# Performance work log

Measured on AMD Instinct MI355X. Metric: run time of the kernel, lower is better.

## Reference

```python
import jax, jax.numpy as jnp
import numpy as np

B, T, H, W, C = 16, 64, 32, 32, 64
DECAY_V = 0.8
VTH_BASE = 0.5

@jax.custom_vjp
def spike_fn(x, alpha):
    return jnp.where(x > 0, 1.0, 0.0)

def _spike_fwd(x, alpha):
    return spike_fn(x, alpha), (x, alpha)

def _spike_bwd(res, g):
    x, alpha = res
    # fast-sigmoid (SuperSpike) surrogate gradient
    surr = 1.0 / (1.0 + alpha * jnp.abs(x)) ** 2
    return (g * surr, jnp.zeros_like(alpha))

spike_fn.defvjp(_spike_fwd, _spike_bwd)


def setup_inputs() -> dict:
    key = jax.random.key(0)
    k0, k1 = jax.random.split(key, 2)
    x = jax.random.normal(k0, (B, T, H, W, C), dtype=jnp.float32)
    # learned params, shapes = x.shape[2:], matching flax initializers
    step_w_raw = jnp.ones((H, W, C), jnp.float32)                      # nn.initializers.ones
    decay_w_raw = 0.1 * jax.random.normal(k1, (H, W, C), jnp.float32)  # normal(stddev=0.1)
    gamma = jnp.ones((H, W, C), jnp.float32)
    beta = jnp.zeros((H, W, C), jnp.float32)
    return {
        "x": x,
        "hp_alpha": jnp.float32(3.0),
        "hp_base_step": jnp.float32(0.1),
        "hp_base_decay": jnp.float32(0.9),
        "step_w_raw": step_w_raw,
        "decay_w_raw": decay_w_raw,
        "gamma": gamma,
        "beta": beta,
    }


def reference(x, hp_alpha, hp_base_step, hp_base_decay, step_w_raw, decay_w_raw, gamma, beta):
    x_seq = jnp.moveaxis(x, 1, 0)  # [T, B, H, W, C]
    step_w = jax.nn.softplus(step_w_raw)
    decay_w = jax.nn.sigmoid(decay_w_raw)
    # time-invariant effective params (hoisted out of scan; same math as original)
    step_eff = hp_base_step * step_w
    decay_eff = hp_base_decay + (1.0 - hp_base_decay) * decay_w

    def scan_fn(state, x_t):
        v, vth_dyn = state
        v = v * DECAY_V + (x_t * gamma + beta)
        vth_eff = VTH_BASE + vth_dyn
        s = spike_fn(v - vth_eff, hp_alpha)
        v_next = v - vth_eff * jax.lax.stop_gradient(s)
        vth_dyn_next = vth_dyn * decay_eff + jax.lax.stop_gradient(s) * step_eff
        return (v_next, vth_dyn_next), (s, v)

    z = jnp.zeros_like(x_seq[0])
    _, (spikes, voltages) = jax.lax.scan(scan_fn, (z, z), x_seq)
    return jnp.moveaxis(spikes, 0, 1), jnp.moveaxis(voltages, 0, 1)
```

## Files before the change

### kernel.cpp

```cpp
#include <hip/hip_runtime.h>
#include <math.h>

constexpr int Bc = 16, Tc = 64, Hc = 32, Wc = 32, Cc = 64;
constexpr int HWC = Hc * Wc * Cc;
constexpr long long NELEM = (long long)Bc * Tc * HWC;
constexpr float DECAY_V = 0.8f;
constexpr float VTH_BASE = 0.5f;

__global__ __launch_bounds__(256) void alif_fwd_kernel(
    const float* __restrict__ x,
    const float* __restrict__ hp_base_step,
    const float* __restrict__ hp_base_decay,
    const float* __restrict__ step_w_raw,
    const float* __restrict__ decay_w_raw,
    const float* __restrict__ gamma,
    const float* __restrict__ beta,
    float* __restrict__ spikes,
    float* __restrict__ volts)
{
    const int tid = blockIdx.x * blockDim.x + threadIdx.x;
    const int c4  = tid << 2;
    const int b   = c4 >> 16;
    const int hwc = c4 & (HWC - 1);

    const float base_step  = *hp_base_step;
    const float base_decay = *hp_base_decay;

    const float4 swr = *(const float4*)(step_w_raw  + hwc);
    const float4 dwr = *(const float4*)(decay_w_raw + hwc);
    const float4 gm4 = *(const float4*)(gamma       + hwc);
    const float4 bt4 = *(const float4*)(beta        + hwc);

    float gm[4]  = {gm4.x, gm4.y, gm4.z, gm4.w};
    float bt[4]  = {bt4.x, bt4.y, bt4.z, bt4.w};
    float swr_a[4] = {swr.x, swr.y, swr.z, swr.w};
    float dwr_a[4] = {dwr.x, dwr.y, dwr.z, dwr.w};

    float step_eff[4], decay_eff[4];
    float v[4]   = {0.f, 0.f, 0.f, 0.f};
    float vth[4] = {0.f, 0.f, 0.f, 0.f};

#pragma unroll
    for (int j = 0; j < 4; ++j) {
        float sw = (float)log1p(exp((double)swr_a[j]));
        float dw = (float)(1.0 / (1.0 + exp(-(double)dwr_a[j])));
        step_eff[j]  = base_step * sw;
        decay_eff[j] = base_decay + (1.0f - base_decay) * dw;
    }

    const size_t base = (size_t)b * Tc * HWC + (size_t)hwc;
    const float* xp = x      + base;
    float*       sp = spikes + base;
    float*       vp = volts  + base;

#pragma unroll 4
    for (int t = 0; t < Tc; ++t) {
        const float4 xv = *(const float4*)xp;
        float xin[4] = {xv.x, xv.y, xv.z, xv.w};
        float4 so, vo;
        float sarr[4], varr[4];
#pragma unroll
        for (int j = 0; j < 4; ++j) {
            float vv      = v[j] * DECAY_V + (xin[j] * gm[j] + bt[j]);
            float vth_eff = VTH_BASE + vth[j];
            float s       = (vv - vth_eff > 0.0f) ? 1.0f : 0.0f;
            varr[j] = vv;
            v[j]    = vv - vth_eff * s;
            vth[j]  = vth[j] * decay_eff[j] + s * step_eff[j];
            sarr[j] = s;
        }
        so.x = sarr[0]; so.y = sarr[1]; so.z = sarr[2]; so.w = sarr[3];
        vo.x = varr[0]; vo.y = varr[1]; vo.z = varr[2]; vo.w = varr[3];
        *(float4*)sp = so;
        *(float4*)vp = vo;
        xp += HWC; sp += HWC; vp += HWC;
    }
}

extern "C" void kernel_launch(void* const* d_in, const int* in_sizes, int n_in,
                              void* d_out, int out_size, void* d_ws, size_t ws_size,
                              hipStream_t stream) {
    const float* x             = (const float*)d_in[0];
    const float* hp_base_step  = (const float*)d_in[2];
    const float* hp_base_decay = (const float*)d_in[3];
    const float* step_w_raw    = (const float*)d_in[4];
    const float* decay_w_raw   = (const float*)d_in[5];
    const float* gamma         = (const float*)d_in[6];
    const float* beta          = (const float*)d_in[7];

    float* spikes = (float*)d_out;
    float* volts  = spikes + NELEM;

    const int threads = 256;
    const int total   = Bc * HWC / 4;
    const int blocks  = total / threads;

    alif_fwd_kernel<<<blocks, threads, 0, stream>>>(
        x, hp_base_step, hp_base_decay, step_w_raw, decay_w_raw,
        gamma, beta, spikes, volts);
}
```

Before: 714.1 us.

## Use float2 per thread with nontemporal loads/stores and one-step x prefetch

Each thread now handles 2 channels instead of 4, doubling thread count to raise memory-level parallelism. Loads and stores of x, spikes and volts use nontemporal builtins to avoid cache pollution for streaming data. The next time step's x is prefetched one iteration ahead, and the unroll factor goes from 4 to 8. The trade-off is narrower 8-byte accesses, which may issue less efficiently than 16-byte ones, plus duplicated per-thread setup work such as the double-precision softplus and sigmoid.

Result: faster. 699.4 us (-2.1%).

```diff
diff --git a/kernel.cpp b/kernel.cpp
--- a/kernel.cpp
+++ b/kernel.cpp
@@ -6,6 +6,8 @@
 constexpr long long NELEM = (long long)Bc * Tc * HWC;
 constexpr float DECAY_V = 0.8f;
 constexpr float VTH_BASE = 0.5f;
+
+typedef float v2f __attribute__((ext_vector_type(2)));
 
 __global__ __launch_bounds__(256) void alif_fwd_kernel(
     const float* __restrict__ x,
@@ -19,29 +21,29 @@
     float* __restrict__ volts)
 {
     const int tid = blockIdx.x * blockDim.x + threadIdx.x;
-    const int c4  = tid << 2;
-    const int b   = c4 >> 16;
-    const int hwc = c4 & (HWC - 1);
+    const int c2  = tid << 1;
+    const int b   = c2 >> 16;
+    const int hwc = c2 & (HWC - 1);
 
     const float base_step  = *hp_base_step;
     const float base_decay = *hp_base_decay;
 
-    const float4 swr = *(const float4*)(step_w_raw  + hwc);
-    const float4 dwr = *(const float4*)(decay_w_raw + hwc);
-    const float4 gm4 = *(const float4*)(gamma       + hwc);
-    const float4 bt4 = *(const float4*)(beta        + hwc);
+    const v2f swr = *(const v2f*)(step_w_raw  + hwc);
+    const v2f dwr = *(const v2f*)(decay_w_raw + hwc);
+    const v2f gm2 = *(const v2f*)(gamma       + hwc);
+    const v2f bt2 = *(const v2f*)(beta        + hwc);
 
-    float gm[4]  = {gm4.x, gm4.y, gm4.z, gm4.w};
-    float bt[4]  = {bt4.x, bt4.y, bt4.z, bt4.w};
-    float swr_a[4] = {swr.x, swr.y, swr.z, swr.w};
-    float dwr_a[4] = {dwr.x, dwr.y, dwr.z, dwr.w};
+    float gm[2]    = {gm2.x, gm2.y};
+    float bt[2]    = {bt2.x, bt2.y};
+    float swr_a[2] = {swr.x, swr.y};
+    float dwr_a[2] = {dwr.x, dwr.y};
 
-    float step_eff[4], decay_eff[4];
-    float v[4]   = {0.f, 0.f, 0.f, 0.f};
-    float vth[4] = {0.f, 0.f, 0.f, 0.f};
+    float step_eff[2], decay_eff[2];
+    float v[2]   = {0.f, 0.f};
+    float vth[2] = {0.f, 0.f};
 
 #pragma unroll
-    for (int j = 0; j < 4; ++j) {
+    for (int j = 0; j < 2; ++j) {
         float sw = (float)log1p(exp((double)swr_a[j]));
         float dw = (float)(1.0 / (1.0 + exp(-(double)dwr_a[j])));
         step_eff[j]  = base_step * sw;
@@ -53,14 +55,17 @@
     float*       sp = spikes + base;
     float*       vp = volts  + base;
 
-#pragma unroll 4
+    v2f xcur = __builtin_nontemporal_load((const v2f*)xp);
+
+#pragma unroll 8
     for (int t = 0; t < Tc; ++t) {
-        const float4 xv = *(const float4*)xp;
-        float xin[4] = {xv.x, xv.y, xv.z, xv.w};
-        float4 so, vo;
-        float sarr[4], varr[4];
+        const float* xnp = xp + ((t + 1 < Tc) ? HWC : 0);
+        v2f xnext = __builtin_nontemporal_load((const v2f*)xnp);
+
+        float xin[2] = {xcur.x, xcur.y};
+        float sarr[2], varr[2];
 #pragma unroll
-        for (int j = 0; j < 4; ++j) {
+        for (int j = 0; j < 2; ++j) {
             float vv      = v[j] * DECAY_V + (xin[j] * gm[j] + bt[j]);
             float vth_eff = VTH_BASE + vth[j];
             float s       = (vv - vth_eff > 0.0f) ? 1.0f : 0.0f;
@@ -69,11 +74,13 @@
             vth[j]  = vth[j] * decay_eff[j] + s * step_eff[j];
             sarr[j] = s;
         }
-        so.x = sarr[0]; so.y = sarr[1]; so.z = sarr[2]; so.w = sarr[3];
-        vo.x = varr[0]; vo.y = varr[1]; vo.z = varr[2]; vo.w = varr[3];
-        *(float4*)sp = so;
-        *(float4*)vp = vo;
-        xp += HWC; sp += HWC; vp += HWC;
+        v2f so = {sarr[0], sarr[1]};
+        v2f vo = {varr[0], varr[1]};
+        __builtin_nontemporal_store(so, (v2f*)sp);
+        __builtin_nontemporal_store(vo, (v2f*)vp);
+
+        xcur = xnext;
+        xp = xnp; sp += HWC; vp += HWC;
     }
 }
 
@@ -92,7 +99,7 @@
     float* volts  = spikes + NELEM;
 
     const int threads = 256;
-    const int total   = Bc * HWC / 4;
+    const int total   = Bc * HWC / 2;
     const int blocks  = total / threads;
 
     alif_fwd_kernel<<<blocks, threads, 0, stream>>>(
```

## Software-pipeline x loads four steps ahead and use nontemporal loads/stores

Applied to the files above, without the earlier changes.

Restructures the time loop so that the next four timesteps of x are loaded into registers while the current four are computed, giving explicit prefetching across the sequential recurrence. It also switches global loads and stores to nontemporal builtins so the streaming data does not pollute the caches. This is meant to hide memory latency in a bandwidth-bound scan. The cost is extra registers for the prefetched vectors.

Result: no change. 710.2 us (-0.5%).

```diff
diff --git a/kernel.cpp b/kernel.cpp
--- a/kernel.cpp
+++ b/kernel.cpp
@@ -6,6 +6,8 @@
 constexpr long long NELEM = (long long)Bc * Tc * HWC;
 constexpr float DECAY_V = 0.8f;
 constexpr float VTH_BASE = 0.5f;
+
+typedef float v4f __attribute__((ext_vector_type(4)));
 
 __global__ __launch_bounds__(256) void alif_fwd_kernel(
     const float* __restrict__ x,
@@ -26,13 +28,13 @@
     const float base_step  = *hp_base_step;
     const float base_decay = *hp_base_decay;
 
-    const float4 swr = *(const float4*)(step_w_raw  + hwc);
-    const float4 dwr = *(const float4*)(decay_w_raw + hwc);
-    const float4 gm4 = *(const float4*)(gamma       + hwc);
-    const float4 bt4 = *(const float4*)(beta        + hwc);
+    const v4f swr = *(const v4f*)(step_w_raw  + hwc);
+    const v4f dwr = *(const v4f*)(decay_w_raw + hwc);
+    const v4f gm4 = *(const v4f*)(gamma       + hwc);
+    const v4f bt4 = *(const v4f*)(beta        + hwc);
 
-    float gm[4]  = {gm4.x, gm4.y, gm4.z, gm4.w};
-    float bt[4]  = {bt4.x, bt4.y, bt4.z, bt4.w};
+    float gm[4]    = {gm4.x, gm4.y, gm4.z, gm4.w};
+    float bt[4]    = {bt4.x, bt4.y, bt4.z, bt4.w};
     float swr_a[4] = {swr.x, swr.y, swr.z, swr.w};
     float dwr_a[4] = {dwr.x, dwr.y, dwr.z, dwr.w};
 
@@ -53,11 +55,8 @@
     float*       sp = spikes + base;
     float*       vp = volts  + base;
 
-#pragma unroll 4
-    for (int t = 0; t < Tc; ++t) {
-        const float4 xv = *(const float4*)xp;
+    auto step = [&](const v4f& xv) {
         float xin[4] = {xv.x, xv.y, xv.z, xv.w};
-        float4 so, vo;
         float sarr[4], varr[4];
 #pragma unroll
         for (int j = 0; j < 4; ++j) {
@@ -69,12 +68,27 @@
             vth[j]  = vth[j] * decay_eff[j] + s * step_eff[j];
             sarr[j] = s;
         }
-        so.x = sarr[0]; so.y = sarr[1]; so.z = sarr[2]; so.w = sarr[3];
-        vo.x = varr[0]; vo.y = varr[1]; vo.z = varr[2]; vo.w = varr[3];
-        *(float4*)sp = so;
-        *(float4*)vp = vo;
-        xp += HWC; sp += HWC; vp += HWC;
+        v4f so = {sarr[0], sarr[1], sarr[2], sarr[3]};
+        v4f vo = {varr[0], varr[1], varr[2], varr[3]};
+        __builtin_nontemporal_store(so, (v4f*)sp);
+        __builtin_nontemporal_store(vo, (v4f*)vp);
+        sp += HWC; vp += HWC;
+    };
+
+#define LDX(off) __builtin_nontemporal_load((const v4f*)(xp + (size_t)(off) * HWC))
+
+    v4f xa = LDX(0), xb = LDX(1), xc = LDX(2), xd = LDX(3);
+    xp += 4 * (size_t)HWC;
+
+    for (int k = 0; k < 15; ++k) {
+        v4f na = LDX(0), nb = LDX(1), nc = LDX(2), nd = LDX(3);
+        xp += 4 * (size_t)HWC;
+        step(xa); step(xb); step(xc); step(xd);
+        xa = na; xb = nb; xc = nc; xd = nd;
     }
+    step(xa); step(xb); step(xc); step(xd);
+
+#undef LDX
 }
 
 extern "C" void kernel_launch(void* const* d_in, const int* in_sizes, int n_in,
```

## Process 16 channels per thread with prefetched x and nontemporal loads/stores

Applied to the files above, without the earlier changes.

Each thread now handles four float4 groups spaced 1024 elements apart, so the grid shrinks from 1024 to 256 blocks. The next timestep's inputs are software-prefetched before the current step is computed, which raises memory-level parallelism per thread. Loads and stores of x, spikes and voltages use nontemporal hints to avoid polluting the cache. The cost is fewer threads in flight: 256 blocks on a GPU with many CUs leaves occupancy low, which may hurt latency hiding on this bandwidth-bound stream.

Result: slower. 752.5 us (+5.4%).

```diff
diff --git a/kernel.cpp b/kernel.cpp
--- a/kernel.cpp
+++ b/kernel.cpp
@@ -6,6 +6,8 @@
 constexpr long long NELEM = (long long)Bc * Tc * HWC;
 constexpr float DECAY_V = 0.8f;
 constexpr float VTH_BASE = 0.5f;
+
+typedef float v4f __attribute__((ext_vector_type(4)));
 
 __global__ __launch_bounds__(256) void alif_fwd_kernel(
     const float* __restrict__ x,
@@ -18,63 +20,79 @@
     float* __restrict__ spikes,
     float* __restrict__ volts)
 {
-    const int tid = blockIdx.x * blockDim.x + threadIdx.x;
-    const int c4  = tid << 2;
-    const int b   = c4 >> 16;
-    const int hwc = c4 & (HWC - 1);
+    const int bk  = (int)blockIdx.x;
+    const int b   = bk >> 4;
+    const int seg = (bk & 15) << 12;
+    const int e0  = seg + ((int)threadIdx.x << 2);
 
     const float base_step  = *hp_base_step;
     const float base_decay = *hp_base_decay;
 
-    const float4 swr = *(const float4*)(step_w_raw  + hwc);
-    const float4 dwr = *(const float4*)(decay_w_raw + hwc);
-    const float4 gm4 = *(const float4*)(gamma       + hwc);
-    const float4 bt4 = *(const float4*)(beta        + hwc);
-
-    float gm[4]  = {gm4.x, gm4.y, gm4.z, gm4.w};
-    float bt[4]  = {bt4.x, bt4.y, bt4.z, bt4.w};
-    float swr_a[4] = {swr.x, swr.y, swr.z, swr.w};
-    float dwr_a[4] = {dwr.x, dwr.y, dwr.z, dwr.w};
-
-    float step_eff[4], decay_eff[4];
-    float v[4]   = {0.f, 0.f, 0.f, 0.f};
-    float vth[4] = {0.f, 0.f, 0.f, 0.f};
-
+    v4f gm[4], bt[4], se[4], de[4];
 #pragma unroll
-    for (int j = 0; j < 4; ++j) {
-        float sw = (float)log1p(exp((double)swr_a[j]));
-        float dw = (float)(1.0 / (1.0 + exp(-(double)dwr_a[j])));
-        step_eff[j]  = base_step * sw;
-        decay_eff[j] = base_decay + (1.0f - base_decay) * dw;
+    for (int k = 0; k < 4; ++k) {
+        const int h = e0 + (k << 10);
+        const v4f swr = *(const v4f*)(step_w_raw  + h);
+        const v4f dwr = *(const v4f*)(decay_w_raw + h);
+        gm[k] = *(const v4f*)(gamma + h);
+        bt[k] = *(const v4f*)(beta  + h);
+#pragma unroll
+        for (int j = 0; j < 4; ++j) {
+            float sw = (float)log1p(exp((double)swr[j]));
+            float dw = (float)(1.0 / (1.0 + exp(-(double)dwr[j])));
+            se[k][j] = base_step * sw;
+            de[k][j] = base_decay + (1.0f - base_decay) * dw;
+        }
     }
 
-    const size_t base = (size_t)b * Tc * HWC + (size_t)hwc;
+    v4f v[4], vth[4];
+#pragma unroll
+    for (int k = 0; k < 4; ++k) { v[k] = (v4f)0.f; vth[k] = (v4f)0.f; }
+
+    const size_t base = (size_t)b * Tc * HWC + (size_t)e0;
     const float* xp = x      + base;
     float*       sp = spikes + base;
     float*       vp = volts  + base;
 
-#pragma unroll 4
-    for (int t = 0; t < Tc; ++t) {
-        const float4 xv = *(const float4*)xp;
-        float xin[4] = {xv.x, xv.y, xv.z, xv.w};
-        float4 so, vo;
-        float sarr[4], varr[4];
+    auto step_all = [&](const v4f* xc) {
+        v4f so[4], vo[4];
 #pragma unroll
-        for (int j = 0; j < 4; ++j) {
-            float vv      = v[j] * DECAY_V + (xin[j] * gm[j] + bt[j]);
-            float vth_eff = VTH_BASE + vth[j];
-            float s       = (vv - vth_eff > 0.0f) ? 1.0f : 0.0f;
-            varr[j] = vv;
-            v[j]    = vv - vth_eff * s;
-            vth[j]  = vth[j] * decay_eff[j] + s * step_eff[j];
-            sarr[j] = s;
+        for (int k = 0; k < 4; ++k) {
+#pragma unroll
+            for (int j = 0; j < 4; ++j) {
+                float vv      = v[k][j] * DECAY_V + (xc[k][j] * gm[k][j] + bt[k][j]);
+                float vth_eff = VTH_BASE + vth[k][j];
+                float s       = (vv - vth_eff > 0.0f) ? 1.0f : 0.0f;
+                vo[k][j]  = vv;
+                v[k][j]   = vv - vth_eff * s;
+                vth[k][j] = vth[k][j] * de[k][j] + s * se[k][j];
+                so[k][j]  = s;
+            }
         }
-        so.x = sarr[0]; so.y = sarr[1]; so.z = sarr[2]; so.w = sarr[3];
-        vo.x = varr[0]; vo.y = varr[1]; vo.z = varr[2]; vo.w = varr[3];
-        *(float4*)sp = so;
-        *(float4*)vp = vo;
-        xp += HWC; sp += HWC; vp += HWC;
+#pragma unroll
+        for (int k = 0; k < 4; ++k)
+            __builtin_nontemporal_store(so[k], (v4f*)(sp + (k << 10)));
+#pragma unroll
+        for (int k = 0; k < 4; ++k)
+            __builtin_nontemporal_store(vo[k], (v4f*)(vp + (k << 10)));
+        sp += HWC; vp += HWC;
+    };
+
+    v4f xc[4], xn[4];
+#pragma unroll
+    for (int k = 0; k < 4; ++k)
+        xc[k] = __builtin_nontemporal_load((const v4f*)(xp + (k << 10)));
+
+    for (int t = 0; t < Tc - 1; ++t) {
+        xp += HWC;
+#pragma unroll
+        for (int k = 0; k < 4; ++k)
+            xn[k] = __builtin_nontemporal_load((const v4f*)(xp + (k << 10)));
+        step_all(xc);
+#pragma unroll
+        for (int k = 0; k < 4; ++k) xc[k] = xn[k];
     }
+    step_all(xc);
 }
 
 extern "C" void kernel_launch(void* const* d_in, const int* in_sizes, int n_in,
@@ -92,8 +110,7 @@
     float* volts  = spikes + NELEM;
 
     const int threads = 256;
-    const int total   = Bc * HWC / 4;
-    const int blocks  = total / threads;
+    const int blocks  = Bc * HWC / (threads * 16);
 
     alif_fwd_kernel<<<blocks, threads, 0, stream>>>(
         x, hp_base_step, hp_base_decay, step_w_raw, decay_w_raw,
```
